# Kernel optimization log

Measured on AMD Instinct MI355X. Metric: run time of the kernel, lower is better.

Reference implementation:

```python
import jax, jax.numpy as jnp
import numpy as np

H = 1024
B_DIM = 64  # bottleneck
EPS = 1e-5

def setup_inputs() -> dict:
    key = jax.random.key(0)
    ks = jax.random.split(key, 5)
    x = jax.random.normal(ks[0], (8, 4096, H), dtype=jnp.float32)
    norm_w = jnp.ones((H,), jnp.float32)
    norm_b = jnp.zeros((H,), jnp.float32)
    # nn.Linear default init ~ U(-1/sqrt(fan_in), 1/sqrt(fan_in))
    lim_d = 1.0 / np.sqrt(H)
    down_w = jax.random.uniform(ks[1], (B_DIM, H), jnp.float32, -lim_d, lim_d)
    down_b = jax.random.uniform(ks[2], (B_DIM,), jnp.float32, -lim_d, lim_d)
    # NOTE: original inits up to zeros; we use small random values so the
    # computation (and gradients) are non-degenerate for kernel testing.
    lim_u = 1.0 / np.sqrt(B_DIM)
    up_w = jax.random.uniform(ks[3], (H, B_DIM), jnp.float32, -lim_u, lim_u)
    up_b = jax.random.uniform(ks[4], (H,), jnp.float32, -lim_u, lim_u)
    return {"x": x, "norm_w": norm_w, "norm_b": norm_b,
            "down_w": down_w, "down_b": down_b, "up_w": up_w, "up_b": up_b}

def reference(x, norm_w, norm_b, down_w, down_b, up_w, up_b):
    # LayerNorm over last dim, eps=1e-5 (PyTorch default)
    mu = jnp.mean(x, axis=-1, keepdims=True)
    var = jnp.mean(jnp.square(x - mu), axis=-1, keepdims=True)
    xn = (x - mu) * jax.lax.rsqrt(var + EPS) * norm_w + norm_b
    # down-proj [B,S,H] @ [H,b] -> [B,S,b]
    h = jnp.einsum('bsh,dh->bsd', xn, down_w) + down_b
    h = jax.nn.gelu(h, approximate=False)  # torch nn.GELU default = exact erf
    # up-proj [B,S,b] @ [b,H] -> [B,S,H], residual add
    out = jnp.einsum('bsd,hd->bsh', h, up_w) + up_b
    return x + out
```

## Files before the change

### kernel.cpp

```cpp
#include <hip/hip_runtime.h>


#define HDIM 1024
#define BDIM 64

using s16x8 = __attribute__((ext_vector_type(8))) short;
using f32x4 = __attribute__((ext_vector_type(4))) float;

__device__ float g_wstat[128];

__device__ __forceinline__ short f2bf(float f) {
  unsigned u = __builtin_bit_cast(unsigned, f);
  u += 0x7fffu + ((u >> 16) & 1u);
  return (short)(u >> 16);
}
__device__ __forceinline__ float bf2f(short s) {
  unsigned u = ((unsigned)(unsigned short)s) << 16;
  return __builtin_bit_cast(float, u);
}

extern "C" __global__ void prep_weights(const float* __restrict__ dw,
                                        const float* __restrict__ uw,
                                        const float* __restrict__ nw,
                                        const float* __restrict__ nb,
                                        const float* __restrict__ db,
                                        short* __restrict__ wsbf) {
  const int b = blockIdx.x;
  if (b < 64) {
    int tid = b * 256 + threadIdx.x;
    if (tid < 8192) {
      int off = tid * 8;
      int k = off & (HDIM - 1);
      f32x4 v0 = *(const f32x4*)(dw + off);
      f32x4 v1 = *(const f32x4*)(dw + off + 4);
      f32x4 g0 = *(const f32x4*)(nw + k);
      f32x4 g1 = *(const f32x4*)(nw + k + 4);
      s16x8 o;
#pragma unroll
      for (int j = 0; j < 4; ++j) {
        o[j]     = f2bf(v0[j] * g0[j]);
        o[j + 4] = f2bf(v1[j] * g1[j]);
      }
      *(s16x8*)(wsbf + tid * 8) = o;
    } else {
      int off = (tid - 8192) * 8;
      f32x4 v0 = *(const f32x4*)(uw + off);
      f32x4 v1 = *(const f32x4*)(uw + off + 4);
      s16x8 o;
#pragma unroll
      for (int j = 0; j < 4; ++j) { o[j] = f2bf(v0[j]); o[j + 4] = f2bf(v1[j]); }
      *(s16x8*)(wsbf + tid * 8) = o;
    }
  } else {
    const int t = threadIdx.x;
    const int n = t >> 2, p = t & 3;
    const float* dwn = dw + n * HDIM;
    float s1 = 0.f, s2 = 0.f;
    for (int j = 0; j < 32; ++j) {
      int k = p * 256 + j * 8;
      f32x4 v0 = *(const f32x4*)(dwn + k);
      f32x4 v1 = *(const f32x4*)(dwn + k + 4);
      f32x4 g0 = *(const f32x4*)(nw + k);
      f32x4 g1 = *(const f32x4*)(nw + k + 4);
      f32x4 b0 = *(const f32x4*)(nb + k);
      f32x4 b1 = *(const f32x4*)(nb + k + 4);
#pragma unroll
      for (int jj = 0; jj < 4; ++jj) {
        s1 += bf2f(f2bf(v0[jj] * g0[jj])) + bf2f(f2bf(v1[jj] * g1[jj]));
        s2 += v0[jj] * b0[jj] + v1[jj] * b1[jj];
      }
    }
    s1 += __shfl_xor(s1, 1); s1 += __shfl_xor(s1, 2);
    s2 += __shfl_xor(s2, 1); s2 += __shfl_xor(s2, 2);
    if (p == 0) {
      g_wstat[n]      = s1;
      g_wstat[64 + n] = db[n] + s2;
    }
  }
}

extern "C" __global__ __launch_bounds__(256, 6)
void adapter_fused(const float* __restrict__ x,
                   const float* __restrict__ ub,
                   const short* __restrict__ dwb,
                   const short* __restrict__ uwb,
                   float* __restrict__ out)
{
  __shared__ __align__(16) float part[4][64][20];
  __shared__ float ssum[4][16];
  __shared__ float sssq[4][16];
  __shared__ __align__(16) short g[16][72];

  const int t    = threadIdx.x;
  const int w    = t >> 6;
  const int lane = t & 63;
  const int q    = lane >> 4;
  const int c    = lane & 15;
  const size_t rowbase = (size_t)blockIdx.x * 16;

  const float* pA  = x   + (rowbase + c) * HDIM + w * 256 + q * 8;
  const short* pB0 = dwb + (size_t)( 0 + c) * HDIM + w * 256 + q * 8;
  const short* pB1 = dwb + (size_t)(16 + c) * HDIM + w * 256 + q * 8;
  const short* pB2 = dwb + (size_t)(32 + c) * HDIM + w * 256 + q * 8;
  const short* pB3 = dwb + (size_t)(48 + c) * HDIM + w * 256 + q * 8;

  f32x4 acc0 = {0.f,0.f,0.f,0.f}, acc1 = acc0, acc2 = acc0, acc3 = acc0;
  float sum = 0.f, ssq = 0.f;

#pragma unroll
  for (int ks = 0; ks < 8; ++ks) {
    f32x4 v0 = *(const f32x4*)(pA + ks * 32);
    f32x4 v1 = *(const f32x4*)(pA + ks * 32 + 4);
    s16x8 b0 = *(const s16x8*)(pB0 + ks * 32);
    s16x8 b1 = *(const s16x8*)(pB1 + ks * 32);
    s16x8 b2 = *(const s16x8*)(pB2 + ks * 32);
    s16x8 b3 = *(const s16x8*)(pB3 + ks * 32);
    s16x8 a;
#pragma unroll
    for (int j = 0; j < 4; ++j) {
      float f0 = v0[j]; sum += f0; ssq += f0 * f0; a[j]     = f2bf(f0);
      float f1 = v1[j]; sum += f1; ssq += f1 * f1; a[j + 4] = f2bf(f1);
    }
    acc0 = __builtin_amdgcn_mfma_f32_16x16x32_bf16(a, b0, acc0, 0, 0, 0);
    acc1 = __builtin_amdgcn_mfma_f32_16x16x32_bf16(a, b1, acc1, 0, 0, 0);
    acc2 = __builtin_amdgcn_mfma_f32_16x16x32_bf16(a, b2, acc2, 0, 0, 0);
    acc3 = __builtin_amdgcn_mfma_f32_16x16x32_bf16(a, b3, acc3, 0, 0, 0);
  }

  sum += __shfl_xor(sum, 16); sum += __shfl_xor(sum, 32);
  ssq += __shfl_xor(ssq, 16); ssq += __shfl_xor(ssq, 32);
  if (lane < 16) { ssum[w][c] = sum; sssq[w][c] = ssq; }

  *(f32x4*)&part[w][ 0 + c][q * 4] = acc0;
  *(f32x4*)&part[w][16 + c][q * 4] = acc1;
  *(f32x4*)&part[w][32 + c][q * 4] = acc2;
  *(f32x4*)&part[w][48 + c][q * 4] = acc3;

  __syncthreads();

  {
    const int n = w * 16 + c;
    f32x4 p0 = *(const f32x4*)&part[0][n][q * 4];
    f32x4 p1 = *(const f32x4*)&part[1][n][q * 4];
    f32x4 p2 = *(const f32x4*)&part[2][n][q * 4];
    f32x4 p3 = *(const f32x4*)&part[3][n][q * 4];
    f32x4 h4 = (p0 + p1) + (p2 + p3);

    const int rr = lane & 15;
    float sT = (ssum[0][rr] + ssum[1][rr]) + (ssum[2][rr] + ssum[3][rr]);
    float qT = (sssq[0][rr] + sssq[1][rr]) + (sssq[2][rr] + sssq[3][rr]);
    const float muL = sT * (1.0f / HDIM);
    const float rsL = rsqrtf(qT * (1.0f / HDIM) - muL * muL + 1e-5f);

    const float sdw = g_wstat[n];
    const float dbv = g_wstat[64 + n];
#pragma unroll
    for (int i = 0; i < 4; ++i) {
      const float m  = __shfl(muL, q * 4 + i);
      const float rv = __shfl(rsL, q * 4 + i);
      float h = rv * (h4[i] - m * sdw) + dbv;
      g[q * 4 + i][n] = f2bf(0.5f * h * (1.0f + erff(h * 0.70710678118654752f)));
    }
  }
  __syncthreads();

  const s16x8 a0 = *(const s16x8*)&g[c][q * 8];
  const s16x8 a1 = *(const s16x8*)&g[c][32 + q * 8];

  const float* xr0 = x + (rowbase + q * 4 + 0) * HDIM + w * 256 + c;
  const float* xr1 = x + (rowbase + q * 4 + 1) * HDIM + w * 256 + c;
  const float* xr2 = x + (rowbase + q * 4 + 2) * HDIM + w * 256 + c;
  const float* xr3 = x + (rowbase + q * 4 + 3) * HDIM + w * 256 + c;
  float* or0 = out + (rowbase + q * 4 + 0) * HDIM + w * 256 + c;
  float* or1 = out + (rowbase + q * 4 + 1) * HDIM + w * 256 + c;
  float* or2 = out + (rowbase + q * 4 + 2) * HDIM + w * 256 + c;
  float* or3 = out + (rowbase + q * 4 + 3) * HDIM + w * 256 + c;
  const short* pu = uwb + (size_t)(w * 256 + c) * BDIM + q * 8;
  const float* pub = ub + w * 256 + c;

#pragma unroll 4
  for (int nt = 0; nt < 16; ++nt) {
    const short* uwrow = pu + (size_t)nt * 16 * BDIM;
    s16x8 b0 = *(const s16x8*)(uwrow);
    s16x8 b1 = *(const s16x8*)(uwrow + 32);
    f32x4 o4 = {0.f,0.f,0.f,0.f};
    o4 = __builtin_amdgcn_mfma_f32_16x16x32_bf16(a0, b0, o4, 0, 0, 0);
    o4 = __builtin_amdgcn_mfma_f32_16x16x32_bf16(a1, b1, o4, 0, 0, 0);
    const float ubv = pub[nt * 16];
    const int co = nt * 16;
    or0[co] = o4[0] + ubv + xr0[co];
    or1[co] = o4[1] + ubv + xr1[co];
    or2[co] = o4[2] + ubv + xr2[co];
    or3[co] = o4[3] + ubv + xr3[co];
  }
}

extern "C" void kernel_launch(void* const* d_in, const int* in_sizes, int n_in,
                              void* d_out, int out_size, void* d_ws, size_t ws_size,
                              hipStream_t stream) {
  const float* x  = (const float*)d_in[0];
  const float* nw = (const float*)d_in[1];
  const float* nb = (const float*)d_in[2];
  const float* dw = (const float*)d_in[3];
  const float* db = (const float*)d_in[4];
  const float* uw = (const float*)d_in[5];
  const float* ub = (const float*)d_in[6];
  float* out = (float*)d_out;

  short* wsbf = (short*)d_ws;
  prep_weights<<<65, 256, 0, stream>>>(dw, uw, nw, nb, db, wsbf);

  const int rows = in_sizes[0] / HDIM;
  const int grid = rows / 16;
  adapter_fused<<<grid, 256, 0, stream>>>(x, ub, wsbf, wsbf + 65536, out);
}
```

Before: 318.5 us.

## Stage bf16 x tile in swizzled LDS and split down-proj by output columns

The first phase now loads each 16-row x tile with coalesced vector reads and converts it to bf16 into a 32KB XOR-swizzled LDS buffer. It computes LayerNorm mean and rstd per row at the same time. The down-projection is then split so each wave owns 16 output columns over the full K from LDS, instead of each wave owning a K-slice and reducing partials through shared memory. This drops the partial-sum reduction and improves global load coalescing, but the larger LDS footprint lowers occupancy (launch bounds go from 6 to 4) and adds LDS traffic.

Measured after the change: 299.5 us. -6.0%, faster.

```diff
diff --git a/kernel.cpp b/kernel.cpp
--- a/kernel.cpp
+++ b/kernel.cpp
@@ -5,6 +5,7 @@
 #define BDIM 64
 
 using s16x8 = __attribute__((ext_vector_type(8))) short;
+using s16x4 = __attribute__((ext_vector_type(4))) short;
 using f32x4 = __attribute__((ext_vector_type(4))) float;
 
 __device__ float g_wstat[128];
@@ -79,16 +80,16 @@
   }
 }
 
-extern "C" __global__ __launch_bounds__(256, 6)
+extern "C" __global__ __launch_bounds__(256, 4)
 void adapter_fused(const float* __restrict__ x,
                    const float* __restrict__ ub,
                    const short* __restrict__ dwb,
                    const short* __restrict__ uwb,
                    float* __restrict__ out)
 {
-  __shared__ __align__(16) float part[4][64][20];
-  __shared__ float ssum[4][16];
-  __shared__ float sssq[4][16];
+  __shared__ __align__(16) short xbf[16 * 1024];
+  __shared__ float muL[16];
+  __shared__ float rsL[16];
   __shared__ __align__(16) short g[16][72];
 
   const int t    = threadIdx.x;
@@ -98,68 +99,58 @@
   const int c    = lane & 15;
   const size_t rowbase = (size_t)blockIdx.x * 16;
 
-  const float* pA  = x   + (rowbase + c) * HDIM + w * 256 + q * 8;
-  const short* pB0 = dwb + (size_t)( 0 + c) * HDIM + w * 256 + q * 8;
-  const short* pB1 = dwb + (size_t)(16 + c) * HDIM + w * 256 + q * 8;
-  const short* pB2 = dwb + (size_t)(32 + c) * HDIM + w * 256 + q * 8;
-  const short* pB3 = dwb + (size_t)(48 + c) * HDIM + w * 256 + q * 8;
-
-  f32x4 acc0 = {0.f,0.f,0.f,0.f}, acc1 = acc0, acc2 = acc0, acc3 = acc0;
-  float sum = 0.f, ssq = 0.f;
-
-#pragma unroll
-  for (int ks = 0; ks < 8; ++ks) {
-    f32x4 v0 = *(const f32x4*)(pA + ks * 32);
-    f32x4 v1 = *(const f32x4*)(pA + ks * 32 + 4);
-    s16x8 b0 = *(const s16x8*)(pB0 + ks * 32);
-    s16x8 b1 = *(const s16x8*)(pB1 + ks * 32);
-    s16x8 b2 = *(const s16x8*)(pB2 + ks * 32);
-    s16x8 b3 = *(const s16x8*)(pB3 + ks * 32);
-    s16x8 a;
-#pragma unroll
-    for (int j = 0; j < 4; ++j) {
-      float f0 = v0[j]; sum += f0; ssq += f0 * f0; a[j]     = f2bf(f0);
-      float f1 = v1[j]; sum += f1; ssq += f1 * f1; a[j + 4] = f2bf(f1);
-    }
-    acc0 = __builtin_amdgcn_mfma_f32_16x16x32_bf16(a, b0, acc0, 0, 0, 0);
-    acc1 = __builtin_amdgcn_mfma_f32_16x16x32_bf16(a, b1, acc1, 0, 0, 0);
-    acc2 = __builtin_amdgcn_mfma_f32_16x16x32_bf16(a, b2, acc2, 0, 0, 0);
-    acc3 = __builtin_amdgcn_mfma_f32_16x16x32_bf16(a, b3, acc3, 0, 0, 0);
-  }
-
-  sum += __shfl_xor(sum, 16); sum += __shfl_xor(sum, 32);
-  ssq += __shfl_xor(ssq, 16); ssq += __shfl_xor(ssq, 32);
-  if (lane < 16) { ssum[w][c] = sum; sssq[w][c] = ssq; }
-
-  *(f32x4*)&part[w][ 0 + c][q * 4] = acc0;
-  *(f32x4*)&part[w][16 + c][q * 4] = acc1;
-  *(f32x4*)&part[w][32 + c][q * 4] = acc2;
-  *(f32x4*)&part[w][48 + c][q * 4] = acc3;
-
+  {
+    const int r  = t >> 4;
+    const int c2 = t & 15;
+    const float* xrow = x + (rowbase + r) * HDIM;
+
+    f32x4 v[16];
+#pragma unroll
+    for (int i = 0; i < 16; ++i) v[i] = ((const f32x4*)xrow)[i * 16 + c2];
+
+    float sum = 0.f, ssq = 0.f;
+#pragma unroll
+    for (int i = 0; i < 16; ++i) {
+      s16x4 o;
+#pragma unroll
+      for (int k = 0; k < 4; ++k) {
+        float f = v[i][k]; sum += f; ssq += f * f; o[k] = f2bf(f);
+      }
+      int b = (i * 128 + c2 * 8) ^ ((r & 7) << 4);
+      *(s16x4*)((char*)xbf + r * 2048 + b) = o;
+    }
+#pragma unroll
+    for (int m = 1; m < 16; m <<= 1) {
+      sum += __shfl_xor(sum, m);
+      ssq += __shfl_xor(ssq, m);
+    }
+    if (c2 == 0) {
+      float mu = sum * (1.0f / HDIM);
+      muL[r] = mu;
+      rsL[r] = rsqrtf(ssq * (1.0f / HDIM) - mu * mu + 1e-5f);
+    }
+  }
   __syncthreads();
 
   {
-    const int n = w * 16 + c;
-    f32x4 p0 = *(const f32x4*)&part[0][n][q * 4];
-    f32x4 p1 = *(const f32x4*)&part[1][n][q * 4];
-    f32x4 p2 = *(const f32x4*)&part[2][n][q * 4];
-    f32x4 p3 = *(const f32x4*)&part[3][n][q * 4];
-    f32x4 h4 = (p0 + p1) + (p2 + p3);
-
-    const int rr = lane & 15;
-    float sT = (ssum[0][rr] + ssum[1][rr]) + (ssum[2][rr] + ssum[3][rr]);
-    float qT = (sssq[0][rr] + sssq[1][rr]) + (sssq[2][rr] + sssq[3][rr]);
-    const float muL = sT * (1.0f / HDIM);
-    const float rsL = rsqrtf(qT * (1.0f / HDIM) - muL * muL + 1e-5f);
-
-    const float sdw = g_wstat[n];
-    const float dbv = g_wstat[64 + n];
+    const short* pB = dwb + (size_t)(w * 16 + c) * HDIM + q * 8;
+    const char*  arow = (const char*)xbf + c * 2048;
+    const int    sw   = (c & 7) << 4;
+    f32x4 acc = {0.f, 0.f, 0.f, 0.f};
+#pragma unroll 8
+    for (int ks = 0; ks < 32; ++ks) {
+      s16x8 a = *(const s16x8*)(arow + ((ks * 64 + q * 16) ^ sw));
+      s16x8 b = *(const s16x8*)(pB + ks * 32);
+      acc = __builtin_amdgcn_mfma_f32_16x16x32_bf16(a, b, acc, 0, 0, 0);
+    }
+
+    const float sdw = g_wstat[w * 16 + c];
+    const float dbv = g_wstat[64 + w * 16 + c];
 #pragma unroll
     for (int i = 0; i < 4; ++i) {
-      const float m  = __shfl(muL, q * 4 + i);
-      const float rv = __shfl(rsL, q * 4 + i);
-      float h = rv * (h4[i] - m * sdw) + dbv;
-      g[q * 4 + i][n] = f2bf(0.5f * h * (1.0f + erff(h * 0.70710678118654752f)));
+      const int m = q * 4 + i;
+      float h = rsL[m] * (acc[i] - muL[m] * sdw) + dbv;
+      g[m][w * 16 + c] = f2bf(0.5f * h * (1.0f + erff(h * 0.70710678118654752f)));
     }
   }
   __syncthreads();
@@ -175,7 +166,7 @@
   float* or1 = out + (rowbase + q * 4 + 1) * HDIM + w * 256 + c;
   float* or2 = out + (rowbase + q * 4 + 2) * HDIM + w * 256 + c;
   float* or3 = out + (rowbase + q * 4 + 3) * HDIM + w * 256 + c;
-  const short* pu = uwb + (size_t)(w * 256 + c) * BDIM + q * 8;
+  const short* pu  = uwb + (size_t)(w * 256 + c) * BDIM + q * 8;
   const float* pub = ub + w * 256 + c;
 
 #pragma unroll 4
@@ -183,7 +174,7 @@
     const short* uwrow = pu + (size_t)nt * 16 * BDIM;
     s16x8 b0 = *(const s16x8*)(uwrow);
     s16x8 b1 = *(const s16x8*)(uwrow + 32);
-    f32x4 o4 = {0.f,0.f,0.f,0.f};
+    f32x4 o4 = {0.f, 0.f, 0.f, 0.f};
     o4 = __builtin_amdgcn_mfma_f32_16x16x32_bf16(a0, b0, o4, 0, 0, 0);
     o4 = __builtin_amdgcn_mfma_f32_16x16x32_bf16(a1, b1, o4, 0, 0, 0);
     const float ubv = pub[nt * 16];
```
